# Kernel optimization log

Measured on AMD Instinct MI355X. Metric: run time of the kernel, lower is better.

Reference implementation:

```python
import math
import jax, jax.numpy as jnp
import numpy as np

B, S, DIN, D, H, FF, L = 128, 200, 2, 512, 8, 2048, 6
HD = D // H
MAXLEN = 201
EPS = 1e-5


def _make_pe():
    den = np.exp(np.arange(0, D, 2) * -math.log(10000.0) / D)
    pos = np.arange(0, MAXLEN).reshape(MAXLEN, 1)
    pe = np.zeros((MAXLEN, D), dtype=np.float32)
    pe[:, 0::2] = np.sin(pos * den)
    pe[:, 1::2] = np.cos(pos * den)
    return jnp.asarray(pe)


def setup_inputs() -> dict:
    key = jax.random.key(0)
    ks = jax.random.split(key, 24)
    r = lambda k, shape: (jax.random.normal(k, shape) * 0.02).astype(jnp.float32)
    z = lambda shape: jnp.zeros(shape, jnp.float32)
    o = lambda shape: jnp.ones(shape, jnp.float32)
    return {
        "traj_o": jax.random.normal(ks[0], (B, S, DIN), jnp.float32),
        "src_padding_mask": jnp.ones((B, S), jnp.int32),
        "pe": _make_pe(),
        "W_emb": r(ks[1], (DIN, D)), "b_emb": z((D,)),
        "Wq": r(ks[2], (L, D, D)), "bq": z((L, D)),
        "Wk": r(ks[3], (L, D, D)), "bk": z((L, D)),
        "Wv": r(ks[4], (L, D, D)), "bv": z((L, D)),
        "Wo": r(ks[5], (L, D, D)), "bo": z((L, D)),
        "ln1_g": o((L, D)), "ln1_b": z((L, D)),
        "W1": r(ks[6], (L, D, FF)), "b1": z((L, FF)),
        "W2": r(ks[7], (L, FF, D)), "b2": z((L, D)),
        "ln2_g": o((L, D)), "ln2_b": z((L, D)),
        "lnf_g": o((D,)), "lnf_b": z((D,)),
    }


def _ln(x, g, b):
    m = jnp.mean(x, axis=-1, keepdims=True)
    v = jnp.var(x, axis=-1, keepdims=True)
    return (x - m) * jax.lax.rsqrt(v + EPS) * g + b


def _forward(traj_o, mask, pe, W_emb, b_emb, Wq, bq, Wk, bk, Wv, bv, Wo, bo,
             ln1_g, ln1_b, W1, b1, W2, b2, ln2_g, ln2_b, lnf_g, lnf_b):
    b, s, _ = traj_o.shape
    x = traj_o @ W_emb + b_emb                         # [B,S,D]
    # faithful to original: adds the single position-s PE vector to all tokens
    x = x + pe[s]                                      # broadcast [D]
    scale = 1.0 / math.sqrt(HD)
    mask4 = (mask[:, None, None, :] == 0)              # [B,1,1,S]
    for i in range(L):
        def proj(W, bias):
            h = x @ W[i] + bias[i]
            return h.reshape(b, s, H, HD).transpose(0, 2, 1, 3)  # [B,H,S,hd]
        q, k, v = proj(Wq, bq), proj(Wk, bk), proj(Wv, bv)
        scores = jnp.einsum('bhqd,bhkd->bhqk', q, k) * scale
        scores = jnp.where(mask4, -jnp.inf, scores)
        probs = jax.nn.softmax(scores, axis=-1)
        ctx = jnp.einsum('bhqk,bhkd->bhqd', probs, v)
        ctx = ctx.transpose(0, 2, 1, 3).reshape(b, s, D)
        attn = ctx @ Wo[i] + bo[i]
        x = _ln(x + attn, ln1_g[i], ln1_b[i])
        ff = jax.nn.relu(x @ W1[i] + b1[i]) @ W2[i] + b2[i]
        x = _ln(x + ff, ln2_g[i], ln2_b[i])
    return _ln(x, lnf_g, lnf_b)


def reference(traj_o, src_padding_mask, pe, W_emb, b_emb, Wq, bq, Wk, bk, Wv, bv,
              Wo, bo, ln1_g, ln1_b, W1, b1, W2, b2, ln2_g, ln2_b, lnf_g, lnf_b):
    return _forward(traj_o, src_padding_mask, pe, W_emb, b_emb, Wq, bq, Wk, bk,
                    Wv, bv, Wo, bo, ln1_g, ln1_b, W1, b1, W2, b2, ln2_g, ln2_b,
                    lnf_g, lnf_b)
```

## Files before the change

kernel.cpp:

```cpp
#include <hip/hip_runtime.h>

typedef unsigned short u16;
typedef __bf16 bf16x8 __attribute__((ext_vector_type(8)));
typedef float f32x4 __attribute__((ext_vector_type(4)));

#define DEV __device__ __forceinline__

DEV u16 f2b(float f){
  union { float f; unsigned u; } v; v.f = f;
  unsigned r = v.u + 0x7FFFu + ((v.u >> 16) & 1u);
  return (u16)(r >> 16);
}
DEV float b2f(u16 h){
  union { unsigned u; float f; } v; v.u = ((unsigned)h) << 16; return v.f;
}

DEV f32x4 zero4(){ f32x4 z; z[0]=0.f; z[1]=0.f; z[2]=0.f; z[3]=0.f; return z; }

DEV void gload16(const u16* g, const u16* l){
  __builtin_amdgcn_global_load_lds(
      (const __attribute__((address_space(1))) unsigned int*)g,
      (__attribute__((address_space(3))) unsigned int*)l, 16, 0, 0);
}

template<int K, int N, long long DSTR>
__global__ __launch_bounds__(256) void transpose_k(const float* __restrict__ src,
                                                   u16* __restrict__ dst){
  __shared__ float tile[32][33];
  const int z = blockIdx.z;
  const float* s = src + (size_t)z*K*N;
  u16* d = dst + (size_t)z*DSTR;
  const int k0 = blockIdx.x*32, n0 = blockIdx.y*32;
  const int tx = threadIdx.x & 31, ty = threadIdx.x >> 5;
  #pragma unroll
  for (int j=0;j<32;j+=8) tile[ty+j][tx] = s[(size_t)(k0+ty+j)*N + n0+tx];
  __syncthreads();
  #pragma unroll
  for (int j=0;j<32;j+=8) d[(size_t)(n0+ty+j)*K + k0+tx] = f2b(tile[tx][ty+j]);
}

__global__ __launch_bounds__(256) void concat_bias(const float* __restrict__ bq,
    const float* __restrict__ bk, const float* __restrict__ bv,
    float* __restrict__ bcat){
  int i = blockIdx.x*256 + threadIdx.x;
  int l = i / 1536, c = i % 1536;
  float v = (c < 512) ? bq[l*512 + c]
          : (c < 1024) ? bk[l*512 + c - 512]
                       : bv[l*512 + c - 1024];
  bcat[i] = v;
}

__global__ __launch_bounds__(256) void embed_kernel(const float* __restrict__ traj,
    const float* __restrict__ We, const float* __restrict__ be,
    const float* __restrict__ pe, u16* __restrict__ xb){
  size_t i = (size_t)blockIdx.x*256 + threadIdx.x;
  int d = (int)(i & 511); size_t tk = i >> 9;
  float v = traj[tk*2]*We[d] + traj[tk*2+1]*We[512+d] + be[d] + pe[200*512 + d];
  xb[i] = f2b(v);
}

template<int K, int NTI, bool RELU>
__global__ __launch_bounds__(512, 2) void gemm256(const u16* __restrict__ A,
    const u16* __restrict__ Bt, const float* __restrict__ bias,
    u16* __restrict__ outp, int nwg){
  constexpr int N = NTI*256;
  constexpr int NT = K/64;
  __shared__ __align__(16) u16 S[65536];
  const int t = threadIdx.x, lane = t&63, w = t>>6;
  const int l16 = lane&15, g16 = lane>>4;
  const int wm = w>>2, wn = w&3;

  const int orig = blockIdx.x;
  const int qq = nwg>>3, rr = nwg&7, xc = orig&7, oo = orig>>3;
  const int wg = (xc<rr ? xc*(qq+1) : rr*(qq+1)+(xc-rr)*qq) + oo;
  const int mt = wg / NTI, ntl = wg % NTI;
  const size_t m0 = (size_t)mt*256, n0 = (size_t)ntl*256;
  const u16* Ab = A + m0*K;
  const u16* Bb = Bt + n0*K;

  const int srow = t>>3;
  const int scol = 8*((t&7) ^ ((t>>3)&7));
  const int kx = (l16&7)<<3;

  f32x4 acc[8][4];
  #pragma unroll
  for (int i=0;i<8;i++)
    #pragma unroll
    for (int j=0;j<4;j++) acc[i][j] = zero4();

  #define STG(g, kb, region, half)                                          \
    { const u16* s0_ = (g) + (size_t)((half)*128 + srow)*K + (kb) + scol;   \
      const u16* s1_ = (g) + (size_t)((half)*128 + 64 + srow)*K + (kb) + scol; \
      gload16(s0_, &S[(region) + (half)*8192 + w*512]);                     \
      gload16(s1_, &S[(region) + (half)*8192 + 4096 + w*512]); }

  STG(Ab, 0, 0, 0);      STG(Ab, 0, 0, 1);
  STG(Bb, 0, 16384, 0);  STG(Bb, 0, 16384, 1);
  STG(Bb, 64, 49152, 0); STG(Bb, 64, 49152, 1);
  asm volatile("s_waitcnt vmcnt(4)" ::: "memory");
  __builtin_amdgcn_s_barrier();

  bf16x8 breg[4][2];

  #define PHASE(AB, BB, Q, LOADB, STG_STMT, VMW)                            \
  {                                                                         \
    bf16x8 af[2][2];                                                        \
    _Pragma("unroll")                                                       \
    for (int j=0;j<2;j++){                                                  \
      _Pragma("unroll")                                                     \
      for (int ks=0;ks<2;ks++)                                              \
        af[j][ks] = *(const bf16x8*)&S[(AB) + (wm*128 + (2*(Q)+j)*16 + l16)*64 \
                                        + ((ks*32 + g16*8) ^ kx)];          \
    }                                                                       \
    if (LOADB){                                                             \
      _Pragma("unroll")                                                     \
      for (int ni=0;ni<4;ni++){                                             \
        _Pragma("unroll")                                                   \
        for (int ks=0;ks<2;ks++)                                            \
          breg[ni][ks] = *(const bf16x8*)&S[(BB) + (wn*64 + ni*16 + l16)*64 \
                                             + ((ks*32 + g16*8) ^ kx)];     \
      }                                                                     \
    }                                                                       \
    STG_STMT;                                                               \
    __builtin_amdgcn_s_barrier();                                           \
    asm volatile("s_waitcnt lgkmcnt(0)" ::: "memory");                      \
    __builtin_amdgcn_sched_barrier(0);                                      \
    __builtin_amdgcn_s_setprio(1);                                          \
    _Pragma("unroll")                                                       \
    for (int ks=0;ks<2;ks++){                                               \
      _Pragma("unroll")                                                     \
      for (int j=0;j<2;j++){                                                \
        _Pragma("unroll")                                                   \
        for (int ni=0;ni<4;ni++)                                            \
          acc[2*(Q)+j][ni] = __builtin_amdgcn_mfma_f32_16x16x32_bf16(       \
              af[j][ks], breg[ni][ks], acc[2*(Q)+j][ni], 0, 0, 0);          \
      }                                                                     \
    }                                                                       \
    __builtin_amdgcn_s_setprio(0);                                          \
    VMW;                                                                    \
    __builtin_amdgcn_s_barrier();                                           \
  }

  for (int it=0; it<NT/2; ++it){
    const int k1 = 2*it+1;
    int k2 = 2*it+2; if (k2 >= NT) k2 -= 2;
    int k3 = 2*it+3; if (k3 >= NT) k3 -= 2;
    PHASE(0,     16384, 0, true,  STG(Ab, k1*64, 32768, 0), ((void)0));
    PHASE(0,     16384, 1, false, STG(Ab, k1*64, 32768, 1), ((void)0));
    PHASE(0,     16384, 2, false, STG(Bb, k2*64, 16384, 0), ((void)0));
    PHASE(0,     16384, 3, false, STG(Bb, k2*64, 16384, 1),
          asm volatile("s_waitcnt vmcnt(4)" ::: "memory"));
    PHASE(32768, 49152, 0, true,  STG(Ab, k2*64, 0, 0), ((void)0));
    PHASE(32768, 49152, 1, false, STG(Ab, k2*64, 0, 1), ((void)0));
    PHASE(32768, 49152, 2, false, STG(Bb, k3*64, 49152, 0), ((void)0));
    PHASE(32768, 49152, 3, false, STG(Bb, k3*64, 49152, 1),
          asm volatile("s_waitcnt vmcnt(4)" ::: "memory"));
  }
  #undef PHASE
  #undef STG

  asm volatile("s_waitcnt vmcnt(0)" ::: "memory");
  __syncthreads();
  float bs[4];
  #pragma unroll
  for (int ni=0;ni<4;ni++) bs[ni] = bias[n0 + wn*64 + ni*16 + l16];
  constexpr int LDE = 264;
  #pragma unroll
  for (int pass=0; pass<2; ++pass){
    const int miB = pass*4;
    #pragma unroll
    for (int miL=0; miL<4; miL++){
      #pragma unroll
      for (int ni=0;ni<4;ni++){
        #pragma unroll
        for (int i=0;i<4;i++){
          float vv = acc[miB+miL][ni][i] + bs[ni];
          if constexpr (RELU) vv = fmaxf(vv, 0.f);
          S[(wm*64 + miL*16 + 4*g16 + i)*LDE + wn*64 + ni*16 + l16] = f2b(vv);
        }
      }
    }
    __syncthreads();
    #pragma unroll
    for (int cc=0; cc<8; cc++){
      const int c = t + cc*512;
      const int R = c >> 5, ck = c & 31;
      uint4 v = *(const uint4*)&S[R*LDE + ck*8];
      const size_t grow = m0 + (size_t)(R>>6)*128 + miB*16 + (R&63);
      *(uint4*)&outp[grow*N + n0 + ck*8] = v;
    }
    if (pass == 0) __syncthreads();
  }
}

__global__ __launch_bounds__(256) void attn_kernel(const u16* __restrict__ qkv,
    const int* __restrict__ mask, u16* __restrict__ ctx){
  __shared__ __align__(16) u16 Vt[64*232];
  __shared__ __align__(16) u16 Ps[4*16*232];
  __shared__ float maskadd[208];
  const int bh = blockIdx.x, b = bh>>3, h = bh&7;
  const int t = threadIdx.x, lane = t&63, w = t>>6;
  const int g16 = lane>>4, l16 = lane&15;

  for (int i=t; i<1856; i+=256) ((uint4*)Vt)[i] = make_uint4(0,0,0,0);
  for (int i=t; i<1856; i+=256) ((uint4*)Ps)[i] = make_uint4(0,0,0,0);
  __syncthreads();

  for (int idx = t; idx < 1600; idx += 256){
    const int s = idx >> 3, d0 = (idx & 7) * 8;
    uint4 v4 = *(const uint4*)&qkv[((size_t)(b*200+s))*1536 + 1024 + h*64 + d0];
    const u16* e = (const u16*)&v4;
    #pragma unroll
    for (int j=0;j<8;j++) Vt[(d0+j)*232 + s] = e[j];
  }
  if (t < 208) maskadd[t] = (t < 200 && mask[b*200+t] != 0) ? 0.f : -1e30f;
  __syncthreads();

  u16* Pw = Ps + w*16*232;
  const float scale = 0.125f;

  for (int rt = w; rt < 13; rt += 4){
    const int rbase = rt*16;
    f32x4 sc[13];
    #pragma unroll
    for (int ct=0;ct<13;ct++) sc[ct] = zero4();

    #pragma unroll
    for (int ks=0; ks<64; ks+=32){
      const int ko = ks + 8*g16;
      const size_t qrow = (size_t)(b*200) + rbase + l16;
      bf16x8 aq = *(const bf16x8*)&qkv[qrow*1536 + h*64 + ko];
      #pragma unroll
      for (int ct=0; ct<13; ct++){
        const size_t krow = (size_t)(b*200) + ct*16 + l16;
        bf16x8 bk8 = *(const bf16x8*)&qkv[krow*1536 + 512 + h*64 + ko];
        sc[ct] = __builtin_amdgcn_mfma_f32_16x16x32_bf16(aq, bk8, sc[ct], 0,0,0);
      }
    }

    float mx[4] = {-1e30f,-1e30f,-1e30f,-1e30f};
    #pragma unroll
    for (int ct=0;ct<13;ct++){
      float ma = maskadd[ct*16 + l16];
      #pragma unroll
      for (int i=0;i<4;i++){
        float s0 = sc[ct][i]*scale + ma;
        sc[ct][i] = s0;
        mx[i] = fmaxf(mx[i], s0);
      }
    }
    #pragma unroll
    for (int i=0;i<4;i++)
      for (int d=1; d<16; d<<=1) mx[i] = fmaxf(mx[i], __shfl_xor(mx[i], d));
    float sm[4] = {0.f,0.f,0.f,0.f};
    #pragma unroll
    for (int ct=0;ct<13;ct++)
      #pragma unroll
      for (int i=0;i<4;i++){
        float e = __expf(sc[ct][i] - mx[i]);
        sc[ct][i] = e; sm[i] += e;
      }
    #pragma unroll
    for (int i=0;i<4;i++)
      for (int d=1; d<16; d<<=1) sm[i] += __shfl_xor(sm[i], d);
    float rs[4];
    #pragma unroll
    for (int i=0;i<4;i++) rs[i] = 1.f/sm[i];

    #pragma unroll
    for (int ct=0;ct<13;ct++)
      #pragma unroll
      for (int i=0;i<4;i++)
        Pw[(4*g16+i)*232 + ct*16 + l16] = f2b(sc[ct][i]);
    asm volatile("s_waitcnt lgkmcnt(0)" ::: "memory");

    f32x4 cacc[4];
    #pragma unroll
    for (int ni=0;ni<4;ni++) cacc[ni] = zero4();
    #pragma unroll
    for (int kt=0; kt<7; kt++){
      const int ko = kt*32 + 8*g16;
      bf16x8 ap = *(const bf16x8*)&Pw[l16*232 + ko];
      #pragma unroll
      for (int ni=0; ni<4; ni++){
        bf16x8 bv8 = *(const bf16x8*)&Vt[(ni*16 + l16)*232 + ko];
        cacc[ni] = __builtin_amdgcn_mfma_f32_16x16x32_bf16(ap, bv8, cacc[ni], 0,0,0);
      }
    }
    #pragma unroll
    for (int ni=0;ni<4;ni++)
      #pragma unroll
      for (int i=0;i<4;i++){
        const int r = rbase + 4*g16 + i;
        if (r < 200)
          ctx[((size_t)(b*200+r))*512 + h*64 + ni*16 + l16] = f2b(cacc[ni][i]*rs[i]);
      }
  }
}

template<bool RESID, bool F32OUT>
__global__ __launch_bounds__(256) void add_ln_bf(const u16* __restrict__ xin,
    const u16* __restrict__ yin, const float* __restrict__ gam,
    const float* __restrict__ bet, u16* __restrict__ bfout,
    float* __restrict__ fout){
  const int r = blockIdx.x*4 + (threadIdx.x>>6);
  const int lane = threadIdx.x & 63;
  const size_t base = (size_t)r*512 + lane*8;
  uint4 xv = *(const uint4*)&xin[base];
  const u16* xp = (const u16*)&xv;
  float vv[8];
  #pragma unroll
  for (int j=0;j<8;j++) vv[j] = b2f(xp[j]);
  if constexpr (RESID){
    uint4 yv = *(const uint4*)&yin[base];
    const u16* yp = (const u16*)&yv;
    #pragma unroll
    for (int j=0;j<8;j++) vv[j] += b2f(yp[j]);
  }
  float s=0.f, q2=0.f;
  #pragma unroll
  for (int j=0;j<8;j++){ s += vv[j]; q2 += vv[j]*vv[j]; }
  #pragma unroll
  for (int d=1; d<64; d<<=1){ s += __shfl_xor(s,d); q2 += __shfl_xor(q2,d); }
  const float mean = s * (1.f/512.f);
  const float var  = q2 * (1.f/512.f) - mean*mean;
  const float rstd = rsqrtf(var + 1e-5f);
  const int col = lane*8;
  float4 g0 = *(const float4*)&gam[col], g1 = *(const float4*)&gam[col+4];
  float4 b0 = *(const float4*)&bet[col], b1 = *(const float4*)&bet[col+4];
  float gg[8] = {g0.x,g0.y,g0.z,g0.w,g1.x,g1.y,g1.z,g1.w};
  float bb[8] = {b0.x,b0.y,b0.z,b0.w,b1.x,b1.y,b1.z,b1.w};
  float o[8];
  #pragma unroll
  for (int j=0;j<8;j++) o[j] = (vv[j]-mean)*rstd*gg[j] + bb[j];
  if constexpr (F32OUT){
    float4 w0 = {o[0],o[1],o[2],o[3]}, w1 = {o[4],o[5],o[6],o[7]};
    *(float4*)&fout[base] = w0;
    *(float4*)&fout[base+4] = w1;
  } else {
    union { u16 pk[8]; uint4 v; } u;
    #pragma unroll
    for (int j=0;j<8;j++) u.pk[j] = f2b(o[j]);
    *(uint4*)&bfout[base] = u.v;
  }
}

extern "C" void kernel_launch(void* const* d_in, const int* in_sizes, int n_in,
                              void* d_out, int out_size, void* d_ws, size_t ws_size,
                              hipStream_t stream){
  const float* traj = (const float*)d_in[0];
  const int*   mask = (const int*)  d_in[1];
  const float* pe   = (const float*)d_in[2];
  const float* We   = (const float*)d_in[3];
  const float* be   = (const float*)d_in[4];
  const float* Wq   = (const float*)d_in[5];
  const float* bq   = (const float*)d_in[6];
  const float* Wk   = (const float*)d_in[7];
  const float* bk   = (const float*)d_in[8];
  const float* Wv   = (const float*)d_in[9];
  const float* bv   = (const float*)d_in[10];
  const float* Wo   = (const float*)d_in[11];
  const float* bo   = (const float*)d_in[12];
  const float* ln1g = (const float*)d_in[13];
  const float* ln1b = (const float*)d_in[14];
  const float* W1   = (const float*)d_in[15];
  const float* b1   = (const float*)d_in[16];
  const float* W2   = (const float*)d_in[17];
  const float* b2   = (const float*)d_in[18];
  const float* ln2g = (const float*)d_in[19];
  const float* ln2b = (const float*)d_in[20];
  const float* lnfg = (const float*)d_in[21];
  const float* lnfb = (const float*)d_in[22];

  const size_t PROJ = 512*512, FFW = (size_t)512*2048, TOK = (size_t)25600*512;
  const size_t QKVW = (size_t)1536*512;
  u16* Wcat = (u16*)d_ws;
  u16* Wot  = Wcat + 6*QKVW;
  u16* W1t  = Wot + 6*PROJ;
  u16* W2t  = W1t + 6*FFW;
  u16* xs   = W2t + 6*FFW;
  u16* R    = xs + TOK;
  u16* qkvb = R;
  u16* ffb  = R;
  u16* cb   = R + (size_t)25600*2048;
  u16* yb   = cb + TOK;
  float* bcat = (float*)(yb + TOK);

  dim3 B256(256);
  transpose_k<512,512,(long long)1536*512><<<dim3(16,16,6), B256, 0, stream>>>(Wq, Wcat);
  transpose_k<512,512,(long long)1536*512><<<dim3(16,16,6), B256, 0, stream>>>(Wk, Wcat + 512*512);
  transpose_k<512,512,(long long)1536*512><<<dim3(16,16,6), B256, 0, stream>>>(Wv, Wcat + 1024*512);
  transpose_k<512,512,(long long)512*512> <<<dim3(16,16,6), B256, 0, stream>>>(Wo, Wot);
  transpose_k<512,2048,(long long)512*2048><<<dim3(16,64,6), B256, 0, stream>>>(W1, W1t);
  transpose_k<2048,512,(long long)512*2048><<<dim3(64,16,6), B256, 0, stream>>>(W2, W2t);
  concat_bias<<<36, B256, 0, stream>>>(bq, bk, bv, bcat);

  embed_kernel<<<51200, B256, 0, stream>>>(traj, We, be, pe, xs);

  for (int i=0; i<6; i++){
    gemm256<512,6,false><<<600, 512, 0, stream>>>(xs, Wcat + (size_t)i*QKVW, bcat + i*1536, qkvb, 600);
    attn_kernel<<<1024, B256, 0, stream>>>(qkvb, mask, cb);
    gemm256<512,2,false><<<200, 512, 0, stream>>>(cb, Wot + (size_t)i*PROJ, bo + i*512, yb, 200);
    add_ln_bf<true,false><<<6400, B256, 0, stream>>>(xs, yb, ln1g + i*512, ln1b + i*512, xs, nullptr);
    gemm256<512,8,true><<<800, 512, 0, stream>>>(xs, W1t + (size_t)i*FFW, b1 + i*2048, ffb, 800);
    gemm256<2048,2,false><<<200, 512, 0, stream>>>(ffb, W2t + (size_t)i*FFW, b2 + i*512, yb, 200);
    add_ln_bf<true,false><<<6400, B256, 0, stream>>>(xs, yb, ln2g + i*512, ln2b + i*512, xs, nullptr);
  }
  add_ln_bf<false,true><<<6400, B256, 0, stream>>>(xs, xs, lnfg, lnfb, nullptr, (float*)d_out);
}
```

Measured before the change: 1.694 ms.

## Fuse residual add and LayerNorm into output-projection and FFN2 GEMM epilogues

Adds a gemm_ln kernel in which each block computes a full 128x512 output row tile, so the epilogue can add bias and the residual and apply LayerNorm in place. It replaces the Wo and W2 GEMMs plus their separate add_ln kernels, removing the yb round trip through global memory and two launches per layer. The tradeoff is a grid of only 200 blocks, each holding wide 128x512 accumulators with a different tile shape than gemm256, which may lower occupancy and parallelism. Variance uses E[x^2]-mean^2 in fp32.

Result: slower. 1.994 ms (+17.7%).

```diff
diff --git a/kernel.cpp b/kernel.cpp
--- a/kernel.cpp
+++ b/kernel.cpp
@@ -193,6 +193,141 @@
   }
 }
 
+template<int K>
+__global__ __launch_bounds__(512, 2) void gemm_ln(const u16* __restrict__ A,
+    const u16* __restrict__ Bt, const float* __restrict__ bias,
+    const u16* resid, const float* __restrict__ gam,
+    const float* __restrict__ bet, u16* outx){
+  constexpr int NT = K/32;
+  __shared__ __align__(16) u16 S[61440];
+  const int t = threadIdx.x, lane = t&63, w = t>>6;
+  const int l16 = lane&15, g16 = lane>>4;
+  const int m0 = blockIdx.x*128;
+  const u16* Ab = A + (size_t)m0*K;
+
+  const int srow = t>>2;
+  const int scol = 8*((t&3) ^ ((t>>3)&3));
+  const int kxa = 8*(g16 ^ ((l16>>1)&3));
+
+  f32x4 acc[8][4];
+  #pragma unroll
+  for (int i=0;i<8;i++)
+    #pragma unroll
+    for (int j=0;j<4;j++) acc[i][j] = zero4();
+
+  int aC = 0, aN = 4096, aS = 8192;
+  int bC = 12288, bN = 28672, bS = 45056;
+
+  #define STGA(kb, dst) gload16(Ab + (size_t)srow*K + (kb) + scol, &S[(dst) + w*512])
+  #define STGB(kb, dst, h) gload16(Bt + (size_t)(128*(h)+srow)*K + (kb) + scol, \
+                                   &S[(dst) + (h)*4096 + w*512])
+
+  STGA(0, aC); STGB(0, bC, 0); STGB(0, bC, 1); STGB(0, bC, 2); STGB(0, bC, 3);
+  STGA(32, aN); STGB(32, bN, 0); STGB(32, bN, 1); STGB(32, bN, 2); STGB(32, bN, 3);
+  asm volatile("s_waitcnt vmcnt(5)" ::: "memory");
+  __builtin_amdgcn_s_barrier();
+
+  for (int k=0; k<NT; ++k){
+    const int kk = (k+2 < NT) ? k+2 : k-1;
+    const int kcol = kk*32;
+    bf16x8 bg[4];
+    {
+      bf16x8 af[4];
+      #pragma unroll
+      for (int j=0;j<4;j++)
+        af[j] = *(const bf16x8*)&S[aC + (j*16+l16)*32 + kxa];
+      #pragma unroll
+      for (int n=0;n<4;n++)
+        bg[n] = *(const bf16x8*)&S[bC + (w*64+n*16+l16)*32 + kxa];
+      STGA(kcol, aS); STGB(kcol, bS, 0); STGB(kcol, bS, 1);
+      __builtin_amdgcn_s_barrier();
+      asm volatile("s_waitcnt lgkmcnt(0)" ::: "memory");
+      __builtin_amdgcn_sched_barrier(0);
+      __builtin_amdgcn_s_setprio(1);
+      #pragma unroll
+      for (int j=0;j<4;j++)
+        #pragma unroll
+        for (int n=0;n<4;n++)
+          acc[j][n] = __builtin_amdgcn_mfma_f32_16x16x32_bf16(af[j], bg[n], acc[j][n], 0,0,0);
+      __builtin_amdgcn_s_setprio(0);
+      __builtin_amdgcn_s_barrier();
+    }
+    {
+      bf16x8 af[4];
+      #pragma unroll
+      for (int j=0;j<4;j++)
+        af[j] = *(const bf16x8*)&S[aC + ((4+j)*16+l16)*32 + kxa];
+      STGB(kcol, bS, 2); STGB(kcol, bS, 3);
+      __builtin_amdgcn_s_barrier();
+      asm volatile("s_waitcnt lgkmcnt(0)" ::: "memory");
+      __builtin_amdgcn_sched_barrier(0);
+      __builtin_amdgcn_s_setprio(1);
+      #pragma unroll
+      for (int j=0;j<4;j++)
+        #pragma unroll
+        for (int n=0;n<4;n++)
+          acc[4+j][n] = __builtin_amdgcn_mfma_f32_16x16x32_bf16(af[j], bg[n], acc[4+j][n], 0,0,0);
+      __builtin_amdgcn_s_setprio(0);
+      asm volatile("s_waitcnt vmcnt(5)" ::: "memory");
+      __builtin_amdgcn_s_barrier();
+    }
+    int ta=aC; aC=aN; aN=aS; aS=ta;
+    int tb=bC; bC=bN; bN=bS; bS=tb;
+  }
+  #undef STGA
+  #undef STGB
+
+  asm volatile("s_waitcnt vmcnt(0)" ::: "memory");
+  __syncthreads();
+  float bs[4];
+  #pragma unroll
+  for (int n=0;n<4;n++) bs[n] = bias[w*64 + n*16 + l16];
+  constexpr int LDE = 520;
+  const int erow = t>>3;
+  const int ec0 = (t&7)*64;
+  #pragma unroll
+  for (int pass=0; pass<2; ++pass){
+    #pragma unroll
+    for (int mi=0; mi<4; mi++)
+      #pragma unroll
+      for (int n=0;n<4;n++)
+        #pragma unroll
+        for (int i=0;i<4;i++)
+          S[(mi*16+4*g16+i)*LDE + w*64 + n*16 + l16] = f2b(acc[pass*4+mi][n][i] + bs[n]);
+    __syncthreads();
+    const size_t grow = (size_t)(m0 + pass*64 + erow);
+    float s1 = 0.f, s2 = 0.f;
+    for (int cc=0; cc<8; ++cc){
+      uint4 lv = *(const uint4*)&S[erow*LDE + ec0 + cc*8];
+      uint4 xv = *(const uint4*)&resid[grow*512 + ec0 + cc*8];
+      const u16* lp = (const u16*)&lv; const u16* xp = (const u16*)&xv;
+      #pragma unroll
+      for (int e=0;e<8;e++){ float v = b2f(lp[e]) + b2f(xp[e]); s1 += v; s2 += v*v; }
+    }
+    #pragma unroll
+    for (int d=1; d<8; d<<=1){ s1 += __shfl_xor(s1,d); s2 += __shfl_xor(s2,d); }
+    const float mean = s1 * (1.f/512.f);
+    const float rstd = rsqrtf(s2 * (1.f/512.f) - mean*mean + 1e-5f);
+    for (int cc=0; cc<8; ++cc){
+      uint4 lv = *(const uint4*)&S[erow*LDE + ec0 + cc*8];
+      uint4 xv = *(const uint4*)&resid[grow*512 + ec0 + cc*8];
+      float4 g0 = *(const float4*)&gam[ec0+cc*8], g1 = *(const float4*)&gam[ec0+cc*8+4];
+      float4 c0 = *(const float4*)&bet[ec0+cc*8], c1 = *(const float4*)&bet[ec0+cc*8+4];
+      const u16* lp = (const u16*)&lv; const u16* xp = (const u16*)&xv;
+      float gg[8] = {g0.x,g0.y,g0.z,g0.w,g1.x,g1.y,g1.z,g1.w};
+      float bb[8] = {c0.x,c0.y,c0.z,c0.w,c1.x,c1.y,c1.z,c1.w};
+      union { u16 pk[8]; uint4 q; } u;
+      #pragma unroll
+      for (int e=0;e<8;e++){
+        float v = b2f(lp[e]) + b2f(xp[e]);
+        u.pk[e] = f2b((v - mean)*rstd*gg[e] + bb[e]);
+      }
+      *(uint4*)&outx[grow*512 + ec0 + cc*8] = u.q;
+    }
+    if (pass == 0) __syncthreads();
+  }
+}
+
 __global__ __launch_bounds__(256) void attn_kernel(const u16* __restrict__ qkv,
     const int* __restrict__ mask, u16* __restrict__ ctx){
   __shared__ __align__(16) u16 Vt[64*232];
@@ -400,11 +535,11 @@
   for (int i=0; i<6; i++){
     gemm256<512,6,false><<<600, 512, 0, stream>>>(xs, Wcat + (size_t)i*QKVW, bcat + i*1536, qkvb, 600);
     attn_kernel<<<1024, B256, 0, stream>>>(qkvb, mask, cb);
-    gemm256<512,2,false><<<200, 512, 0, stream>>>(cb, Wot + (size_t)i*PROJ, bo + i*512, yb, 200);
-    add_ln_bf<true,false><<<6400, B256, 0, stream>>>(xs, yb, ln1g + i*512, ln1b + i*512, xs, nullptr);
+    gemm_ln<512><<<200, 512, 0, stream>>>(cb, Wot + (size_t)i*PROJ, bo + i*512,
+                                          xs, ln1g + i*512, ln1b + i*512, xs);
     gemm256<512,8,true><<<800, 512, 0, stream>>>(xs, W1t + (size_t)i*FFW, b1 + i*2048, ffb, 800);
-    gemm256<2048,2,false><<<200, 512, 0, stream>>>(ffb, W2t + (size_t)i*FFW, b2 + i*512, yb, 200);
-    add_ln_bf<true,false><<<6400, B256, 0, stream>>>(xs, yb, ln2g + i*512, ln2b + i*512, xs, nullptr);
+    gemm_ln<2048><<<200, 512, 0, stream>>>(ffb, W2t + (size_t)i*FFW, b2 + i*512,
+                                           xs, ln2g + i*512, ln2b + i*512, xs);
   }
   add_ln_bf<false,true><<<6400, B256, 0, stream>>>(xs, xs, lnfg, lnfb, nullptr, (float*)d_out);
 }
```
